# Kernel optimization log

Measured on AMD Instinct MI355X. Metric: run time of the kernel, lower is better.

The kernel has to match this reference:

```python
import jax, jax.numpy as jnp
import numpy as np

BLK = 32
BIT = 8
BN_EPS = 1e-5


def _ste(x, xq):
    # straight-through estimator: forward = xq, backward = identity
    return x + jax.lax.stop_gradient(xq - x)


def bfp_quant_act(x, bit=BIT, blk=BLK):
    # Block floating point: shared exponent over blocks of `blk` channels
    # at each (n, h, w); mantissa quantized to `bit` bits (incl. sign).
    N, C, H, W = x.shape
    xb = x.reshape(N, C // blk, blk, H, W)
    maxabs = jnp.max(jnp.abs(xb), axis=2, keepdims=True)
    e = jnp.floor(jnp.log2(jnp.maximum(maxabs, 1e-12)))  # shared exponent
    scale = jnp.exp2(e + 1.0 - (bit - 1))
    qmax = 2.0 ** (bit - 1)
    q = jnp.clip(jnp.round(xb / scale), -qmax, qmax - 1.0)
    xq = (q * scale).reshape(N, C, H, W)
    return _ste(x, xq)


def dsconv_weight_quant(w, bit=BIT, blk=BLK):
    # DSConv VQK: per-block (blk input channels, per output channel, per
    # spatial tap) integer quantization with a float per-block scale (KDS).
    O, I, kh, kw = w.shape
    wb = w.reshape(O, I // blk, blk, kh, kw)
    qmax = 2.0 ** (bit - 1) - 1.0
    scale = jnp.maximum(jnp.max(jnp.abs(wb), axis=2, keepdims=True), 1e-12) / qmax
    q = jnp.clip(jnp.round(wb / scale), -qmax - 1.0, qmax)
    wq = (q * scale).reshape(O, I, kh, kw)
    return _ste(w, wq)


def conv2d(x, w, stride, padding):
    return jax.lax.conv_general_dilated(
        x, w, window_strides=(stride, stride),
        padding=[(padding, padding), (padding, padding)],
        dimension_numbers=('NCHW', 'OIHW', 'NCHW'))


def batchnorm(x, g, b, m, v):
    inv = g / jnp.sqrt(v + BN_EPS)
    return x * inv[None, :, None, None] + (b - m * inv)[None, :, None, None]


def setup_inputs() -> dict:
    key = jax.random.key(0)
    ks = jax.random.split(key, 12)
    N, Cin, Cout, H, W = 64, 128, 256, 56, 56
    inp = {
        'x':  jax.random.normal(ks[0], (N, Cin, H, W), jnp.float32),
        'w1': jax.random.normal(ks[1], (Cout, Cin, 3, 3), jnp.float32) * 0.05,
        'w2': jax.random.normal(ks[2], (Cout, Cout, 3, 3), jnp.float32) * 0.05,
        'ws': jax.random.normal(ks[3], (Cout, Cin, 1, 1), jnp.float32) * 0.05,
        'bn1_g': jnp.ones((Cout,), jnp.float32),
        'bn1_b': jnp.zeros((Cout,), jnp.float32),
        'bn1_m': jax.random.normal(ks[4], (Cout,), jnp.float32) * 0.1,
        'bn1_v': jax.random.uniform(ks[5], (Cout,), jnp.float32, 0.5, 1.5),
        'bn2_g': jnp.ones((Cout,), jnp.float32),
        'bn2_b': jnp.zeros((Cout,), jnp.float32),
        'bn2_m': jax.random.normal(ks[6], (Cout,), jnp.float32) * 0.1,
        'bn2_v': jax.random.uniform(ks[7], (Cout,), jnp.float32, 0.5, 1.5),
        'bns_g': jnp.ones((Cout,), jnp.float32),
        'bns_b': jnp.zeros((Cout,), jnp.float32),
        'bns_m': jax.random.normal(ks[8], (Cout,), jnp.float32) * 0.1,
        'bns_v': jax.random.uniform(ks[9], (Cout,), jnp.float32, 0.5, 1.5),
    }
    return inp


def reference(x, w1, w2, ws, bn1_g, bn1_b, bn1_m, bn1_v,
              bn2_g, bn2_b, bn2_m, bn2_v, bns_g, bns_b, bns_m, bns_v):
    stride = 2
    # conv1 (DSConv 3x3, stride 2) -> BN -> ReLU -> BFP activation quant
    out = conv2d(x, dsconv_weight_quant(w1), stride, 1)
    out = jax.nn.relu(batchnorm(out, bn1_g, bn1_b, bn1_m, bn1_v))
    out = bfp_quant_act(out)
    # conv2 (DSConv 3x3, stride 1) -> BN
    out = conv2d(out, dsconv_weight_quant(w2), 1, 1)
    out = batchnorm(out, bn2_g, bn2_b, bn2_m, bn2_v)
    # downsample shortcut: DSConv 1x1 stride 2 -> BN
    sc = conv2d(x, dsconv_weight_quant(ws), stride, 0)
    sc = batchnorm(sc, bns_g, bns_b, bns_m, bns_v)
    out = jax.nn.relu(out + sc)
    out = bfp_quant_act(out)  # activation2 (last=False)
    return out
```

## Files before the change

### kernel.cpp

```cpp
#include <hip/hip_runtime.h>
#include <stdint.h>

typedef unsigned short u16;
typedef __bf16 bf16x8 __attribute__((ext_vector_type(8)));
typedef float f32x4 __attribute__((ext_vector_type(4)));

#define NB    64
#define CIN   128
#define COUT  256
#define PIMG  960
#define MPT   7
#define NMT   448

static constexpr size_t XT4_BYTES = (size_t)64*64*PIMG*8*2;
static constexpr size_t A1C_BYTES = (size_t)32*64*PIMG*8*2;
static constexpr size_t BT1_BYTES = (size_t)2*144*128*8*2;
static constexpr size_t BT2_BYTES = (size_t)2*304*128*8*2;
static constexpr size_t OFF_XT4  = 0;
static constexpr size_t OFF_A1C  = OFF_XT4 + XT4_BYTES;
static constexpr size_t OFF_B1   = OFF_A1C + A1C_BYTES;
static constexpr size_t OFF_B2   = OFF_B1 + BT1_BYTES;
static constexpr size_t OFF_BETA = OFF_B2 + BT2_BYTES;

static __device__ __forceinline__ u16 f2bf(float f) {
  uint32_t u = __float_as_uint(f);
  u += 0x7fffu + ((u >> 16) & 1u);
  return (u16)(u >> 16);
}

typedef const __attribute__((address_space(1))) uint32_t* gas1;
typedef __attribute__((address_space(3))) uint32_t* las3;
static __device__ __forceinline__ void gl16(const void* g, void* l) {
  __builtin_amdgcn_global_load_lds((gas1)(uintptr_t)g,
                                   (las3)(uint32_t)(uintptr_t)l, 16, 0, 0);
}

static __device__ __forceinline__ void quant2(float v0, float v1, float& o0, float& o1) {
  float mx = fmaxf(v0, v1);
  mx = fmaxf(mx, __shfl_xor(mx, 1));
  mx = fmaxf(mx, __shfl_xor(mx, 2));
  mx = fmaxf(mx, __shfl_xor(mx, 4));
  mx = fmaxf(mx, __shfl_xor(mx, 8));
  mx = fmaxf(mx, 1e-12f);
  const int e = (int)(__float_as_uint(mx) >> 23) - 127;
  const float scale = __uint_as_float((uint32_t)(e + 121) << 23);
  const float invs  = __uint_as_float((uint32_t)(133 - e) << 23);
  o0 = fminf(rintf(v0 * invs), 127.f) * scale;
  o1 = fminf(rintf(v1 * invs), 127.f) * scale;
}

__global__ void k_transpose(const float* __restrict__ x, u16* __restrict__ xt4) {
  __shared__ float s[32][33];
  const int ht = blockIdx.x, ct = blockIdx.y, n = blockIdx.z;
  const int t = threadIdx.x, tc = t >> 5, tw = t & 31;
  const float* src = x + ((size_t)(n*CIN + ct*32))*3136 + ht*32;
#pragma unroll
  for (int i = 0; i < 4; ++i)
    s[tc + i*8][tw] = src[(size_t)(tc + i*8)*3136 + tw];
  __syncthreads();
  const int c = ct*32 + tw;
#pragma unroll
  for (int i = 0; i < 4; ++i) {
    const int hwl = tc + i*8;
    const int hw = ht*32 + hwl;
    const int h = hw / 56, w = hw % 56;
    const int py = h + 1, px = w + 1;
    const int sub = (py & 1)*2 + (px & 1);
    const int p = (py >> 1)*32 + (px >> 1);
    xt4[(((size_t)(sub*16 + (c >> 3))*64 + n)*PIMG + p)*8 + (c & 7)]
        = f2bf(s[tw][hwl]);
  }
}

__global__ void k_prep(const float* __restrict__ w1, const float* __restrict__ w2,
                       const float* __restrict__ wsc,
                       const float* __restrict__ g1, const float* __restrict__ b1,
                       const float* __restrict__ m1, const float* __restrict__ v1,
                       const float* __restrict__ g2, const float* __restrict__ b2,
                       const float* __restrict__ m2, const float* __restrict__ v2,
                       const float* __restrict__ gs, const float* __restrict__ bs,
                       const float* __restrict__ ms, const float* __restrict__ vs,
                       u16* __restrict__ B1, u16* __restrict__ B2,
                       float* __restrict__ beta)
{
  const int id = blockIdx.x*256 + threadIdx.x;
  if (id < 9216) {
    const int o = id / 36, rem = id % 36, ib = rem / 9, t = rem % 9;
    const float inv = g1[o] / sqrtf(v1[o] + 1e-5f);
    const float* base = w1 + (size_t)(o*CIN + ib*32)*9 + t;
    float mx = 0.f;
#pragma unroll 8
    for (int jj = 0; jj < 32; ++jj) mx = fmaxf(mx, fabsf(base[jj*9]));
    const float scale = fmaxf(mx, 1e-12f) / 127.0f;
#pragma unroll 8
    for (int jj = 0; jj < 32; ++jj) {
      float q = rintf(base[jj*9] / scale);
      q = fminf(fmaxf(q, -128.f), 127.f);
      const int kc = t*16 + ib*4 + (jj >> 3);
      B1[(((size_t)(o >> 7)*144 + kc)*128 + (o & 127))*8 + (jj & 7)]
          = f2bf(q * scale * inv);
    }
  } else if (id < 27648) {
    const int id2 = id - 9216;
    const int o = id2 / 72, rem = id2 % 72, ib = rem / 9, t = rem % 9;
    const float inv = g2[o] / sqrtf(v2[o] + 1e-5f);
    const float* base = w2 + (size_t)(o*COUT + ib*32)*9 + t;
    float mx = 0.f;
#pragma unroll 8
    for (int jj = 0; jj < 32; ++jj) mx = fmaxf(mx, fabsf(base[jj*9]));
    const float scale = fmaxf(mx, 1e-12f) / 127.0f;
#pragma unroll 8
    for (int jj = 0; jj < 32; ++jj) {
      float q = rintf(base[jj*9] / scale);
      q = fminf(fmaxf(q, -128.f), 127.f);
      const int kc = t*32 + ib*4 + (jj >> 3);
      B2[(((size_t)(o >> 7)*304 + kc)*128 + (o & 127))*8 + (jj & 7)]
          = f2bf(q * scale * inv);
    }
  } else if (id < 28672) {
    const int id3 = id - 27648;
    const int o = id3 >> 2, ib = id3 & 3;
    const float inv = gs[o] / sqrtf(vs[o] + 1e-5f);
    const float* base = wsc + (size_t)o*CIN + ib*32;
    float mx = 0.f;
#pragma unroll 8
    for (int jj = 0; jj < 32; ++jj) mx = fmaxf(mx, fabsf(base[jj]));
    const float scale = fmaxf(mx, 1e-12f) / 127.0f;
#pragma unroll 8
    for (int jj = 0; jj < 32; ++jj) {
      float q = rintf(base[jj] / scale);
      q = fminf(fmaxf(q, -128.f), 127.f);
      const int kc = 288 + ib*4 + (jj >> 3);
      B2[(((size_t)(o >> 7)*304 + kc)*128 + (o & 127))*8 + (jj & 7)]
          = f2bf(q * scale * inv);
    }
  } else if (id < 29184) {
    const int id4 = id - 28672;
    const int which = id4 >> 8, o = id4 & 255;
    if (which == 0) {
      beta[o] = b1[o] - m1[o] * (g1[o] / sqrtf(v1[o] + 1e-5f));
    } else {
      beta[256 + o] = (b2[o] - m2[o] * (g2[o] / sqrtf(v2[o] + 1e-5f)))
                    + (bs[o] - ms[o] * (gs[o] / sqrtf(vs[o] + 1e-5f)));
    }
  }
}

template<int MODE>
__global__ __launch_bounds__(256, 4)
void gemm_k(const u16* __restrict__ Ag, const u16* __restrict__ Ag2,
            const u16* __restrict__ Bg, const float* __restrict__ beta,
            u16* __restrict__ a1c, float* __restrict__ of32)
{
  __shared__ __align__(16) u16 As[2][4][128][8];
  __shared__ __align__(16) u16 Bs[2][4][128][8];

  const int tid = threadIdx.x;
  const int wv  = tid >> 6;
  const int ln  = tid & 63;
  const int b   = blockIdx.x;
  const int xcd = b & 7, j = b >> 3;
  const int mtile = xcd*56 + (j % 56);
  const int ntile = j / 56;

  constexpr int NKA = (MODE == 0) ? 36 : 72;
  constexpr int NK  = (MODE == 0) ? 36 : 76;
  constexpr int NKC = (MODE == 0) ? 144 : 304;
  constexpr int GSH = (MODE == 0) ? 4 : 5;

  const int n  = mtile / MPT;
  const int p0 = (mtile % MPT) * 128;

  const char* const Bb = (const char*)Bg + (size_t)ntile*NKC*2048 + (size_t)ln*16;

  auto issue = [&](int nk, int slot) {
    const int kc = nk*4 + wv;
    const char* a;
    if (MODE == 1 && nk >= NKA) {
      const int g = kc - 288;
      a = (const char*)Ag2 + (((size_t)(48 + g)*64 + n)*PIMG + p0)*16;
    } else if (MODE == 0) {
      const int t = kc >> GSH, g = kc & ((1 << GSH) - 1);
      const int dy = t / 3, dx = t - dy*3;
      const int sub = (dy & 1)*2 + (dx & 1);
      a = (const char*)Ag +
          (((size_t)(sub*16 + g)*64 + n)*PIMG + p0 + (dy >> 1)*32 + (dx >> 1))*16;
    } else {
      const int t = kc >> GSH, g = kc & ((1 << GSH) - 1);
      const int dy = t / 3, dx = t - dy*3;
      a = (const char*)Ag + (((size_t)g*64 + n)*PIMG + p0 + dy*32 + dx)*16;
    }
    a += (size_t)ln*16;
    const char* bb = Bb + (size_t)kc*2048;
    char* la = (char*)&As[slot][wv][0][0];
    char* lb = (char*)&Bs[slot][wv][0][0];
    gl16(a,        la);
    gl16(a + 1024, la + 1024);
    gl16(bb,        lb);
    gl16(bb + 1024, lb + 1024);
  };

  const int quad = ln >> 4, l15 = ln & 15;
  const int m_off = (wv & 1)*64, n_off = (wv >> 1)*64;
  const u16* ra[4];
  const u16* rb[4];
#pragma unroll
  for (int i = 0; i < 4; ++i) {
    ra[i] = As[0][quad][m_off + i*16 + l15];
    rb[i] = Bs[0][quad][n_off + i*16 + l15];
  }

  f32x4 acc[4][4];
#pragma unroll
  for (int i = 0; i < 4; ++i)
#pragma unroll
    for (int j2 = 0; j2 < 4; ++j2)
      acc[i][j2] = (f32x4){0.f, 0.f, 0.f, 0.f};

  issue(0, 0);
  issue(1, 1);

  int buf = 0;
  for (int i = 0; i < NK; ++i) {
    if (i + 1 < NK)      asm volatile("s_waitcnt vmcnt(4)" ::: "memory");
    else                 asm volatile("s_waitcnt vmcnt(0)" ::: "memory");
    asm volatile("s_barrier" ::: "memory");

    const int bsel = buf * 4096;
    bf16x8 av[4], bv[4];
#pragma unroll
    for (int k = 0; k < 4; ++k) av[k] = *(const bf16x8*)(ra[k] + bsel);
#pragma unroll
    for (int k = 0; k < 4; ++k) bv[k] = *(const bf16x8*)(rb[k] + bsel);
#pragma unroll
    for (int mi = 0; mi < 4; ++mi)
#pragma unroll
      for (int ni = 0; ni < 4; ++ni)
        acc[mi][ni] = __builtin_amdgcn_mfma_f32_16x16x32_bf16(av[mi], bv[ni], acc[mi][ni], 0, 0, 0);

    if (i + 2 < NK) {
      asm volatile("s_waitcnt lgkmcnt(0)" ::: "memory");
      asm volatile("s_barrier" ::: "memory");
      issue(i + 2, buf);
    }
    buf ^= 1;
  }

  const int cbase = ntile*128 + n_off;
  const int p0m   = p0 + m_off;
  float bt[4];
#pragma unroll
  for (int ni = 0; ni < 4; ++ni) bt[ni] = beta[cbase + ni*16 + l15];

  if constexpr (MODE == 0) {
#pragma unroll
    for (int mi = 0; mi < 4; ++mi)
#pragma unroll
      for (int r = 0; r < 4; ++r) {
        const int idx = p0m + mi*16 + quad*4 + r;
        if ((idx & 31) < 28) {
          float v[4];
#pragma unroll
          for (int ni = 0; ni < 4; ++ni) v[ni] = fmaxf(acc[mi][ni][r] + bt[ni], 0.f);
#pragma unroll
          for (int g = 0; g < 2; ++g) {
            float o0, o1;
            quant2(v[2*g], v[2*g+1], o0, o1);
            const int c0 = cbase + (2*g)*16 + l15;
            const int c1 = c0 + 16;
            a1c[(((size_t)(c0 >> 3)*64 + n)*PIMG + idx + 33)*8 + (c0 & 7)]
                = (u16)(__float_as_uint(o0) >> 16);
            a1c[(((size_t)(c1 >> 3)*64 + n)*PIMG + idx + 33)*8 + (c1 & 7)]
                = (u16)(__float_as_uint(o1) >> 16);
          }
        }
      }
  } else {
#pragma unroll
    for (int mi = 0; mi < 4; ++mi) {
      float ov[4][4];
#pragma unroll
      for (int r = 0; r < 4; ++r) {
        float v[4];
#pragma unroll
        for (int ni = 0; ni < 4; ++ni)
          v[ni] = fmaxf(acc[mi][ni][r] + bt[ni], 0.f);
#pragma unroll
        for (int g = 0; g < 2; ++g)
          quant2(v[2*g], v[2*g+1], ov[2*g][r], ov[2*g+1][r]);
      }
      const int idx0 = p0m + mi*16 + quad*4;
      const int x0 = idx0 & 31, y = idx0 >> 5;
      if (x0 < 28) {
#pragma unroll
        for (int ni = 0; ni < 4; ++ni) {
          const int c = cbase + ni*16 + l15;
          f32x4 val = { ov[ni][0], ov[ni][1], ov[ni][2], ov[ni][3] };
          *(f32x4*)(of32 + ((size_t)(n*COUT + c)*28 + y)*28 + x0) = val;
        }
      }
    }
  }
}

extern "C" void kernel_launch(void* const* d_in, const int* in_sizes, int n_in,
                              void* d_out, int out_size, void* d_ws, size_t ws_size,
                              hipStream_t stream)
{
  (void)in_sizes; (void)n_in; (void)out_size; (void)ws_size;
  const float* x   = (const float*)d_in[0];
  const float* w1  = (const float*)d_in[1];
  const float* w2  = (const float*)d_in[2];
  const float* wsc = (const float*)d_in[3];
  const float* g1 = (const float*)d_in[4];
  const float* b1 = (const float*)d_in[5];
  const float* m1 = (const float*)d_in[6];
  const float* v1 = (const float*)d_in[7];
  const float* g2 = (const float*)d_in[8];
  const float* b2 = (const float*)d_in[9];
  const float* m2 = (const float*)d_in[10];
  const float* v2 = (const float*)d_in[11];
  const float* gs = (const float*)d_in[12];
  const float* bs = (const float*)d_in[13];
  const float* ms = (const float*)d_in[14];
  const float* vs = (const float*)d_in[15];

  char* ws = (char*)d_ws;
  u16* xt4  = (u16*)(ws + OFF_XT4);
  u16* a1c  = (u16*)(ws + OFF_A1C);
  u16* B1   = (u16*)(ws + OFF_B1);
  u16* B2   = (u16*)(ws + OFF_B2);
  float* beta = (float*)(ws + OFF_BETA);

  hipMemsetAsync(ws, 0, OFF_B1, stream);

  k_transpose<<<dim3(98, 4, 64), 256, 0, stream>>>(x, xt4);
  k_prep<<<114, 256, 0, stream>>>(w1, w2, wsc, g1, b1, m1, v1,
                                  g2, b2, m2, v2, gs, bs, ms, vs,
                                  B1, B2, beta);
  gemm_k<0><<<896, 256, 0, stream>>>(xt4, nullptr, B1, beta, a1c, nullptr);
  gemm_k<1><<<896, 256, 0, stream>>>(a1c, xt4, B2, beta + 256, nullptr, (float*)d_out);
}
```

Baseline: 348.4 us.

## Enlarge GEMM M-tile to 256 and flatten pixel indexing across images

The M tile of both implicit-GEMM kernels grows from 128 to 256 output pixels, so each wave now computes 8x4 MFMA tiles instead of 4x4. The pixel dimension is treated as one flat space across all images, so a tile can straddle an image boundary, and the epilogue maps each pixel back to its image and position. This raises MFMA work per shared-memory load of B and cuts the grid from 896 to 480 blocks, aiming to improve reuse and reduce per-block overhead. In exchange it needs more accumulator registers and LDS, so occupancy is reduced (launch bounds 4 to 2), and some rows are wasted on padding pixels across image boundaries.

After: 355.0 us. About the same (+1.9%).

```diff
diff --git a/kernel.cpp b/kernel.cpp
--- a/kernel.cpp
+++ b/kernel.cpp
@@ -9,11 +9,10 @@
 #define CIN   128
 #define COUT  256
 #define PIMG  960
-#define MPT   7
-#define NMT   448
-
-static constexpr size_t XT4_BYTES = (size_t)64*64*PIMG*8*2;
-static constexpr size_t A1C_BYTES = (size_t)32*64*PIMG*8*2;
+#define PTOT  61440
+
+static constexpr size_t XT4_BYTES = (size_t)64*PTOT*8*2;
+static constexpr size_t A1C_BYTES = (size_t)32*PTOT*8*2;
 static constexpr size_t BT1_BYTES = (size_t)2*144*128*8*2;
 static constexpr size_t BT2_BYTES = (size_t)2*304*128*8*2;
 static constexpr size_t OFF_XT4  = 0;
@@ -147,12 +146,12 @@
 }
 
 template<int MODE>
-__global__ __launch_bounds__(256, 4)
+__global__ __launch_bounds__(256, 2)
 void gemm_k(const u16* __restrict__ Ag, const u16* __restrict__ Ag2,
             const u16* __restrict__ Bg, const float* __restrict__ beta,
             u16* __restrict__ a1c, float* __restrict__ of32)
 {
-  __shared__ __align__(16) u16 As[2][4][128][8];
+  __shared__ __align__(16) u16 As[2][4][256][8];
   __shared__ __align__(16) u16 Bs[2][4][128][8];
 
   const int tid = threadIdx.x;
@@ -160,16 +159,15 @@
   const int ln  = tid & 63;
   const int b   = blockIdx.x;
   const int xcd = b & 7, j = b >> 3;
-  const int mtile = xcd*56 + (j % 56);
-  const int ntile = j / 56;
+  const int mtile = xcd*30 + (j % 30);
+  const int ntile = j / 30;
 
   constexpr int NKA = (MODE == 0) ? 36 : 72;
   constexpr int NK  = (MODE == 0) ? 36 : 76;
   constexpr int NKC = (MODE == 0) ? 144 : 304;
   constexpr int GSH = (MODE == 0) ? 4 : 5;
 
-  const int n  = mtile / MPT;
-  const int p0 = (mtile % MPT) * 128;
+  const int gp0 = mtile * 256;
 
   const char* const Bb = (const char*)Bg + (size_t)ntile*NKC*2048 + (size_t)ln*16;
 
@@ -178,17 +176,17 @@
     const char* a;
     if (MODE == 1 && nk >= NKA) {
       const int g = kc - 288;
-      a = (const char*)Ag2 + (((size_t)(48 + g)*64 + n)*PIMG + p0)*16;
+      a = (const char*)Ag2 + ((size_t)(48 + g)*PTOT + gp0)*16;
     } else if (MODE == 0) {
       const int t = kc >> GSH, g = kc & ((1 << GSH) - 1);
       const int dy = t / 3, dx = t - dy*3;
       const int sub = (dy & 1)*2 + (dx & 1);
       a = (const char*)Ag +
-          (((size_t)(sub*16 + g)*64 + n)*PIMG + p0 + (dy >> 1)*32 + (dx >> 1))*16;
+          ((size_t)(sub*16 + g)*PTOT + gp0 + (dy >> 1)*32 + (dx >> 1))*16;
     } else {
       const int t = kc >> GSH, g = kc & ((1 << GSH) - 1);
       const int dy = t / 3, dx = t - dy*3;
-      a = (const char*)Ag + (((size_t)g*64 + n)*PIMG + p0 + dy*32 + dx)*16;
+      a = (const char*)Ag + ((size_t)g*PTOT + gp0 + dy*32 + dx)*16;
     }
     a += (size_t)ln*16;
     const char* bb = Bb + (size_t)kc*2048;
@@ -196,23 +194,26 @@
     char* lb = (char*)&Bs[slot][wv][0][0];
     gl16(a,        la);
     gl16(a + 1024, la + 1024);
+    gl16(a + 2048, la + 2048);
+    gl16(a + 3072, la + 3072);
     gl16(bb,        lb);
     gl16(bb + 1024, lb + 1024);
   };
 
   const int quad = ln >> 4, l15 = ln & 15;
-  const int m_off = (wv & 1)*64, n_off = (wv >> 1)*64;
-  const u16* ra[4];
+  const int m_off = (wv & 1)*128, n_off = (wv >> 1)*64;
+  const u16* ra[8];
   const u16* rb[4];
 #pragma unroll
-  for (int i = 0; i < 4; ++i) {
+  for (int i = 0; i < 8; ++i)
     ra[i] = As[0][quad][m_off + i*16 + l15];
+#pragma unroll
+  for (int i = 0; i < 4; ++i)
     rb[i] = Bs[0][quad][n_off + i*16 + l15];
-  }
-
-  f32x4 acc[4][4];
-#pragma unroll
-  for (int i = 0; i < 4; ++i)
+
+  f32x4 acc[8][4];
+#pragma unroll
+  for (int i = 0; i < 8; ++i)
 #pragma unroll
     for (int j2 = 0; j2 < 4; ++j2)
       acc[i][j2] = (f32x4){0.f, 0.f, 0.f, 0.f};
@@ -222,18 +223,19 @@
 
   int buf = 0;
   for (int i = 0; i < NK; ++i) {
-    if (i + 1 < NK)      asm volatile("s_waitcnt vmcnt(4)" ::: "memory");
+    if (i + 1 < NK)      asm volatile("s_waitcnt vmcnt(6)" ::: "memory");
     else                 asm volatile("s_waitcnt vmcnt(0)" ::: "memory");
     asm volatile("s_barrier" ::: "memory");
 
-    const int bsel = buf * 4096;
-    bf16x8 av[4], bv[4];
-#pragma unroll
-    for (int k = 0; k < 4; ++k) av[k] = *(const bf16x8*)(ra[k] + bsel);
-#pragma unroll
-    for (int k = 0; k < 4; ++k) bv[k] = *(const bf16x8*)(rb[k] + bsel);
-#pragma unroll
-    for (int mi = 0; mi < 4; ++mi)
+    const int aoff = buf * 8192;
+    const int boff = buf * 4096;
+    bf16x8 av[8], bv[4];
+#pragma unroll
+    for (int k = 0; k < 8; ++k) av[k] = *(const bf16x8*)(ra[k] + aoff);
+#pragma unroll
+    for (int k = 0; k < 4; ++k) bv[k] = *(const bf16x8*)(rb[k] + boff);
+#pragma unroll
+    for (int mi = 0; mi < 8; ++mi)
 #pragma unroll
       for (int ni = 0; ni < 4; ++ni)
         acc[mi][ni] = __builtin_amdgcn_mfma_f32_16x16x32_bf16(av[mi], bv[ni], acc[mi][ni], 0, 0, 0);
@@ -247,18 +249,23 @@
   }
 
   const int cbase = ntile*128 + n_off;
-  const int p0m   = p0 + m_off;
   float bt[4];
 #pragma unroll
   for (int ni = 0; ni < 4; ++ni) bt[ni] = beta[cbase + ni*16 + l15];
 
+  const int gpw = gp0 + m_off;
+  const int n0  = gpw / 960;
+  const int r0  = gpw % 960;
+
   if constexpr (MODE == 0) {
 #pragma unroll
-    for (int mi = 0; mi < 4; ++mi)
+    for (int mi = 0; mi < 8; ++mi)
 #pragma unroll
       for (int r = 0; r < 4; ++r) {
-        const int idx = p0m + mi*16 + quad*4 + r;
-        if ((idx & 31) < 28) {
+        const int lo  = r0 + mi*16 + quad*4 + r;
+        const int loc = (lo >= 960) ? lo - 960 : lo;
+        if (loc < 896 && (loc & 31) < 28) {
+          const int gp = gpw + mi*16 + quad*4 + r;
           float v[4];
 #pragma unroll
           for (int ni = 0; ni < 4; ++ni) v[ni] = fmaxf(acc[mi][ni][r] + bt[ni], 0.f);
@@ -268,16 +275,16 @@
             quant2(v[2*g], v[2*g+1], o0, o1);
             const int c0 = cbase + (2*g)*16 + l15;
             const int c1 = c0 + 16;
-            a1c[(((size_t)(c0 >> 3)*64 + n)*PIMG + idx + 33)*8 + (c0 & 7)]
+            a1c[((size_t)(c0 >> 3)*PTOT + gp + 33)*8 + (c0 & 7)]
                 = (u16)(__float_as_uint(o0) >> 16);
-            a1c[(((size_t)(c1 >> 3)*64 + n)*PIMG + idx + 33)*8 + (c1 & 7)]
+            a1c[((size_t)(c1 >> 3)*PTOT + gp + 33)*8 + (c1 & 7)]
                 = (u16)(__float_as_uint(o1) >> 16);
           }
         }
       }
   } else {
 #pragma unroll
-    for (int mi = 0; mi < 4; ++mi) {
+    for (int mi = 0; mi < 8; ++mi) {
       float ov[4][4];
 #pragma unroll
       for (int r = 0; r < 4; ++r) {
@@ -289,14 +296,16 @@
         for (int g = 0; g < 2; ++g)
           quant2(v[2*g], v[2*g+1], ov[2*g][r], ov[2*g+1][r]);
       }
-      const int idx0 = p0m + mi*16 + quad*4;
-      const int x0 = idx0 & 31, y = idx0 >> 5;
-      if (x0 < 28) {
+      const int lo   = r0 + mi*16 + quad*4;
+      const int nimg = (lo >= 960) ? n0 + 1 : n0;
+      const int loc  = (lo >= 960) ? lo - 960 : lo;
+      const int x0 = loc & 31, y = loc >> 5;
+      if (x0 < 28 && loc < 896) {
 #pragma unroll
         for (int ni = 0; ni < 4; ++ni) {
           const int c = cbase + ni*16 + l15;
           f32x4 val = { ov[ni][0], ov[ni][1], ov[ni][2], ov[ni][3] };
-          *(f32x4*)(of32 + ((size_t)(n*COUT + c)*28 + y)*28 + x0) = val;
+          *(f32x4*)(of32 + ((size_t)(nimg*COUT + c)*28 + y)*28 + x0) = val;
         }
       }
     }
@@ -338,6 +347,6 @@
   k_prep<<<114, 256, 0, stream>>>(w1, w2, wsc, g1, b1, m1, v1,
                                   g2, b2, m2, v2, gs, bs, ms, vs,
                                   B1, B2, beta);
-  gemm_k<0><<<896, 256, 0, stream>>>(xt4, nullptr, B1, beta, a1c, nullptr);
-  gemm_k<1><<<896, 256, 0, stream>>>(a1c, xt4, B2, beta + 256, nullptr, (float*)d_out);
-}
+  gemm_k<0><<<480, 256, 0, stream>>>(xt4, nullptr, B1, beta, a1c, nullptr);
+  gemm_k<1><<<480, 256, 0, stream>>>(a1c, xt4, B2, beta + 256, nullptr, (float*)d_out);
+}
```
